# Kernel tuning notes

Hardware: AMD Instinct MI355X
Metric: run time of the kernel (lower is better)

## Reference

```python
import jax, jax.numpy as jnp
import numpy as np

VOCAB = 32000
DIM = 1024
N_BLOCKS = 5
L_CONST = 1e9


def setup_inputs() -> dict:
    key = jax.random.key(0)
    k1, k2, k3, k4, k5, k6 = jax.random.split(key, 6)
    x = jax.random.normal(k1, (2, 2048, DIM), dtype=jnp.float32)
    gates_w = jax.random.uniform(k2, (VOCAB, 1), dtype=jnp.float32)  # mimics uniform_(0.001, 1.0)
    weight = jax.random.normal(k3, (DIM, VOCAB), dtype=jnp.float32) * 0.02
    bias = jax.random.normal(k4, (VOCAB,), dtype=jnp.float32) * 0.02
    blk_w = jax.random.normal(k5, (N_BLOCKS, DIM, DIM), dtype=jnp.float32) * 0.02
    blk_b = jax.random.normal(k6, (N_BLOCKS, DIM), dtype=jnp.float32) * 0.02
    return {"x": x, "gates_w": gates_w, "weight": weight, "bias": bias, "blk_w": blk_w, "blk_b": blk_b}


def reference(x, gates_w, weight, bias, blk_w, blk_b):
    input_dim, vocab = weight.shape  # [D, V]
    gates = gates_w * input_dim  # [V, 1], scaled per-token gate
    idx = jnp.arange(input_dim, dtype=jnp.float32)[None, :]  # [1, D]
    # discrete mask + straight-through residual term (broadcast [V,1] over [V,D])
    mask = (idx < gates).astype(jnp.float32) + (L_CONST * gates - jnp.floor(L_CONST * gates)) / L_CONST  # [V, D]
    masked_weight = weight * mask.T  # [D, V]
    # branch selector per vocab column, in {0,...,4}
    selector = jnp.floor(gates / x.shape[-1] * N_BLOCKS * (1.0 - 1e-10)).reshape(vocab)  # [V]
    ret = jnp.zeros(x.shape[:-1] + (vocab,), dtype=x.dtype)
    for bidx in range(N_BLOCKS):
        x_b = jnp.einsum('bsd,ed->bse', x, blk_w[bidx]) + blk_b[bidx]  # Linear: x @ W^T + b
        temp = jnp.einsum('bsd,dv->bsv', x_b, masked_weight)  # [B, S, V]
        ret = ret + temp * (selector == bidx).astype(jnp.float32)
    return ret + bias
```

## Files before the change

### kernel.cpp

```cpp
#include <hip/hip_runtime.h>
#include <hip/hip_bf16.h>

#define VOCAB 32000
#define DIM 1024
#define NTOK 4096
#define NG 5
#define MAXTILES 255

typedef float f32x4 __attribute__((ext_vector_type(4)));
typedef __bf16 bf16x8 __attribute__((ext_vector_type(8)));

__device__ __forceinline__ unsigned short f2bf(float f) {
    union { float f; unsigned int u; } x; x.f = f;
    unsigned int r = x.u + 0x7fffu + ((x.u >> 16) & 1u);
    return (unsigned short)(r >> 16);
}
__device__ __forceinline__ float bf2f(unsigned short u) {
    union { unsigned int u; float f; } x; x.u = ((unsigned int)u) << 16;
    return x.f;
}

__device__ __forceinline__ void gload16(const void* g, void* l) {
    __builtin_amdgcn_global_load_lds(
        (const __attribute__((address_space(1))) void*)g,
        (__attribute__((address_space(3))) void*)l, 16, 0, 0);
}

__global__ __launch_bounds__(256) void hist_kernel(const float* __restrict__ gates_w,
                                                   int* __restrict__ hist) {
    __shared__ int cnt[NG];
    const int tid = threadIdx.x;
    if (tid < NG) cnt[tid] = 0;
    __syncthreads();
    const int v = blockIdx.x * 256 + tid;
    const int s = min(4, max(0, (int)floorf(gates_w[v] * 5.0f)));
    atomicAdd(&cnt[s], 1);
    __syncthreads();
    if (tid < NG) hist[blockIdx.x * NG + tid] = cnt[tid];
}

__global__ __launch_bounds__(64) void base_kernel(const int* __restrict__ hist,
                                                  int* __restrict__ blkoff,
                                                  int* __restrict__ jlist,
                                                  int4* __restrict__ tdesc,
                                                  int* __restrict__ pbase6) {
    __shared__ int histl[125 * NG];
    __shared__ int cnt[NG], pb[NG], padc[NG];
    const int tid = threadIdx.x;
    for (int i = tid; i < 125 * NG; i += 64) histl[i] = hist[i];
    __syncthreads();
    if (tid == 0) {
        int c[NG] = {0, 0, 0, 0, 0};
        for (int b = 0; b < 125; ++b)
            for (int g = 0; g < NG; ++g) c[g] += histl[b * NG + g];
        const int kmaxs[NG] = {256, 448, 640, 832, 1024};
        int p = 0, t = 0;
        for (int g = 0; g < NG; ++g) {
            pb[g] = p; cnt[g] = c[g];
            padc[g] = ((c[g] + 127) >> 7) << 7;
            pbase6[g] = p;
            p += padc[g];
        }
        pbase6[NG] = p;
        for (int g = 0; g < NG; ++g) {
            int nt = (cnt[g] + 127) >> 7;
            for (int k = 0; k < nt; ++k) { tdesc[t] = make_int4(g, pb[g] + (k << 7), kmaxs[g], 0); ++t; }
        }
        for (; t < MAXTILES; ++t) tdesc[t] = make_int4(-1, 0, 0, 0);
        int run[NG];
        for (int g = 0; g < NG; ++g) run[g] = pb[g];
        for (int b = 0; b < 125; ++b)
            for (int g = 0; g < NG; ++g) { blkoff[b * NG + g] = run[g]; run[g] += histl[b * NG + g]; }
    }
    __syncthreads();
    for (int g = 0; g < NG; ++g)
        for (int i = pb[g] + cnt[g] + tid; i < pb[g] + padc[g]; i += 64) jlist[i] = -1;
}

__global__ __launch_bounds__(256) void place_kernel(const float* __restrict__ gates_w,
                                                    const int* __restrict__ blkoff,
                                                    int* __restrict__ pos,
                                                    int* __restrict__ jlist) {
    __shared__ int wtot[4][NG], wpre[4][NG];
    const int tid = threadIdx.x, lane = tid & 63, wv = tid >> 6;
    const int v = blockIdx.x * 256 + tid;
    const int s = min(4, max(0, (int)floorf(gates_w[v] * 5.0f)));
    int rank = 0;
#pragma unroll
    for (int g = 0; g < NG; ++g) {
        unsigned long long m = __ballot(s == g);
        if (lane == 0) wtot[wv][g] = (int)__popcll(m);
        if (s == g) rank = (int)__popcll(m & ((1ull << lane) - 1ull));
    }
    __syncthreads();
    if (tid < NG) {
        int a = 0;
        for (int w = 0; w < 4; ++w) { wpre[w][tid] = a; a += wtot[w][tid]; }
    }
    __syncthreads();
    const int p = blkoff[blockIdx.x * NG + s] + wpre[wv][s] + rank;
    pos[v] = p;
    jlist[p] = v;
}

__global__ void conv_kernel(const float* __restrict__ in, unsigned short* __restrict__ out, int n4) {
    int i = blockIdx.x * blockDim.x + threadIdx.x;
    if (i >= n4) return;
    const float4 f = ((const float4*)in)[i];
    ushort4 o;
    o.x = f2bf(f.x); o.y = f2bf(f.y); o.z = f2bf(f.z); o.w = f2bf(f.w);
    ((ushort4*)out)[i] = o;
}

__global__ __launch_bounds__(256) void convT_kernel(const float* __restrict__ blk_w,
                                                    unsigned short* __restrict__ wbfT) {
    __shared__ unsigned short tl[64][68];
    const int i0 = blockIdx.x * 64, o0 = blockIdx.y * 64, g = blockIdx.z;
    const int tid = threadIdx.x;
    const float* src = blk_w + (size_t)g * DIM * DIM;
    unsigned short* dst = wbfT + (size_t)g * DIM * DIM;
#pragma unroll
    for (int it = 0; it < 4; ++it) {
        int idx = it * 256 + tid;
        int lo = idx >> 4;
        int c4 = (idx & 15) * 4;
        float4 w = *(const float4*)&src[(size_t)(o0 + lo) * DIM + i0 + c4];
        tl[c4 + 0][lo] = f2bf(w.x);
        tl[c4 + 1][lo] = f2bf(w.y);
        tl[c4 + 2][lo] = f2bf(w.z);
        tl[c4 + 3][lo] = f2bf(w.w);
    }
    __syncthreads();
#pragma unroll
    for (int it = 0; it < 2; ++it) {
        int idx = it * 256 + tid;
        int ri = idx >> 3, ch = idx & 7;
        union { unsigned short u[8]; uint4 q; } uu;
#pragma unroll
        for (int k = 0; k < 8; ++k) uu.u[k] = tl[ri][ch * 8 + k];
        *(uint4*)(dst + (size_t)(i0 + ri) * DIM + o0 + ch * 8) = uu.q;
    }
}

__global__ __launch_bounds__(256) void wm_kernel(const float* __restrict__ weight,
                                                 const float* __restrict__ gates_w,
                                                 const int* __restrict__ pos,
                                                 unsigned short* __restrict__ wmbp) {
    __shared__ unsigned short tl[64][68];
    __shared__ float gatev[64];
    __shared__ int posv[64];
    const int v0 = blockIdx.x * 64, d0 = blockIdx.y * 64;
    const int tid = threadIdx.x;
    if (tid < 64) { gatev[tid] = gates_w[v0 + tid] * 1024.0f; posv[tid] = pos[v0 + tid]; }
    __syncthreads();
#pragma unroll
    for (int it = 0; it < 4; ++it) {
        int idx = it * 256 + tid;
        int ld = idx >> 4;
        int c4 = (idx & 15) * 4;
        const float dv = (float)(d0 + ld);
        float4 w = *(const float4*)&weight[(size_t)(d0 + ld) * VOCAB + v0 + c4];
        tl[c4 + 0][ld] = f2bf((dv < gatev[c4 + 0]) ? w.x : 0.0f);
        tl[c4 + 1][ld] = f2bf((dv < gatev[c4 + 1]) ? w.y : 0.0f);
        tl[c4 + 2][ld] = f2bf((dv < gatev[c4 + 2]) ? w.z : 0.0f);
        tl[c4 + 3][ld] = f2bf((dv < gatev[c4 + 3]) ? w.w : 0.0f);
    }
    __syncthreads();
#pragma unroll
    for (int it = 0; it < 2; ++it) {
        int idx = it * 256 + tid;
        int lv = idx >> 3, ch = idx & 7;
        union { unsigned short u[8]; uint4 q; } uu;
#pragma unroll
        for (int k = 0; k < 8; ++k) uu.u[k] = tl[lv][ch * 8 + k];
        *(uint4*)(wmbp + (size_t)posv[lv] * DIM + d0 + ch * 8) = uu.q;
    }
}

__global__ __launch_bounds__(256) void dbias_kernel(const unsigned short* __restrict__ wmbp,
                                                    const float* __restrict__ blk_b,
                                                    const float* __restrict__ bias,
                                                    const int* __restrict__ jlist,
                                                    const int* __restrict__ pbase6,
                                                    float* __restrict__ bias2) {
    const int p = blockIdx.x * 4 + (threadIdx.x >> 6);
    const int lane = threadIdx.x & 63;
    if (p >= pbase6[NG]) return;
    const int v = jlist[p];
    if (v < 0) return;
    int g = 0;
#pragma unroll
    for (int gg = 1; gg < NG; ++gg) if (p >= pbase6[gg]) g = gg;
    const unsigned short* wrow = wmbp + (size_t)p * DIM + lane * 16;
    const float* brow = blk_b + g * DIM + lane * 16;
    union { uint4 q; unsigned short u[8]; } a0, a1;
    a0.q = *(const uint4*)(wrow);
    a1.q = *(const uint4*)(wrow + 8);
    float s = 0.f;
#pragma unroll
    for (int k = 0; k < 8; ++k) s += bf2f(a0.u[k]) * brow[k];
#pragma unroll
    for (int k = 0; k < 8; ++k) s += bf2f(a1.u[k]) * brow[k + 8];
#pragma unroll
    for (int off = 32; off > 0; off >>= 1) s += __shfl_down(s, off);
    if (lane == 0) bias2[v] = bias[v] + s;
}

__global__ __launch_bounds__(256, 2) void ceff_gemm(const unsigned short* __restrict__ wmbp,
                                                    const unsigned short* __restrict__ wbfT,
                                                    const int* __restrict__ jlist,
                                                    const int4* __restrict__ tdesc,
                                                    unsigned short* __restrict__ ceffv) {
    const int4 td = tdesc[blockIdx.x];
    if (td.x < 0) return;
    const int g = td.x, jb = td.y, kmax = td.z;
    const int n0 = blockIdx.y * 128;
    __shared__ __align__(16) unsigned short lA[128 * 64];
    __shared__ __align__(16) unsigned short lB[128 * 64];
    const int tid = threadIdx.x;
    const int lane = tid & 63, wv = tid >> 6;
    const int wm64 = (wv >> 1) * 64, wn64 = (wv & 1) * 64;
    const int lr = lane >> 4, lc = lane & 15;
    f32x4 acc[4][4] = {};
    const int r = tid >> 3, c = tid & 7;
    const unsigned short* sa = wmbp + (size_t)(jb + r) * DIM + c * 8;
    const unsigned short* sb = wbfT + (size_t)g * DIM * DIM + (size_t)(n0 + r) * DIM + c * 8;
    unsigned short* da = &lA[r * 64 + c * 8];
    unsigned short* db = &lB[r * 64 + c * 8];
    const int nkt = kmax >> 6;
    for (int kt = 0; kt < nkt; ++kt) {
#pragma unroll
        for (int s = 0; s < 4; ++s) {
            gload16(sa + (size_t)s * 32 * DIM + kt * 64, da + s * 32 * 64);
            gload16(sb + (size_t)s * 32 * DIM + kt * 64, db + s * 32 * 64);
        }
        __syncthreads();
#pragma unroll
        for (int kk = 0; kk < 64; kk += 32) {
            const int ko = kk + lr * 8;
            bf16x8 af[4], bg[4];
#pragma unroll
            for (int m = 0; m < 4; ++m) af[m] = *(const bf16x8*)&lA[(wm64 + m * 16 + lc) * 64 + ko];
#pragma unroll
            for (int n = 0; n < 4; ++n) bg[n] = *(const bf16x8*)&lB[(wn64 + n * 16 + lc) * 64 + ko];
#pragma unroll
            for (int m = 0; m < 4; ++m)
#pragma unroll
                for (int n = 0; n < 4; ++n)
                    acc[m][n] = __builtin_amdgcn_mfma_f32_16x16x32_bf16(af[m], bg[n], acc[m][n], 0, 0, 0);
        }
        __syncthreads();
    }
#pragma unroll
    for (int m = 0; m < 4; ++m) {
#pragma unroll
        for (int i = 0; i < 4; ++i) {
            const int prow = jb + wm64 + m * 16 + lr * 4 + i;
            const int v = jlist[prow];
            if (v < 0) continue;
#pragma unroll
            for (int n = 0; n < 4; ++n) {
                const int icol = n0 + wn64 + n * 16 + lc;
                ceffv[(size_t)v * DIM + icol] = f2bf(acc[m][n][i]);
            }
        }
    }
}

__global__ __launch_bounds__(256, 4) void out_gemm(const unsigned short* __restrict__ xbf,
                                                   const unsigned short* __restrict__ ceffv,
                                                   const float* __restrict__ bias2,
                                                   float* __restrict__ out) {
    const int rid = blockIdx.y * gridDim.x + blockIdx.x;
    const int swz = (rid & 7) * 1000 + (rid >> 3);
    const int m0 = (swz & 31) * 128;
    const int n0 = (swz >> 5) * 128;
    __shared__ __align__(16) unsigned short lA[128 * 64];
    __shared__ __align__(16) unsigned short lB[128 * 64];
    const int tid = threadIdx.x;
    const int lane = tid & 63, wv = tid >> 6;
    const int wm64 = (wv >> 1) * 64, wn64 = (wv & 1) * 64;
    const int lr = lane >> 4, lc = lane & 15;
    f32x4 acc[4][4] = {};
    const int r = tid >> 3, c = tid & 7;
    const unsigned short* sa = xbf + (size_t)(m0 + r) * DIM + c * 8;
    const unsigned short* sb = ceffv + (size_t)(n0 + r) * DIM + c * 8;
    unsigned short* da = &lA[r * 64 + c * 8];
    unsigned short* db = &lB[r * 64 + c * 8];
    for (int kt = 0; kt < DIM / 64; ++kt) {
#pragma unroll
        for (int s = 0; s < 4; ++s) {
            gload16(sa + (size_t)s * 32 * DIM + kt * 64, da + s * 32 * 64);
            gload16(sb + (size_t)s * 32 * DIM + kt * 64, db + s * 32 * 64);
        }
        __syncthreads();
#pragma unroll
        for (int kk = 0; kk < 64; kk += 32) {
            const int ko = kk + lr * 8;
            bf16x8 af[4], bg[4];
#pragma unroll
            for (int m = 0; m < 4; ++m) af[m] = *(const bf16x8*)&lA[(wm64 + m * 16 + lc) * 64 + ko];
#pragma unroll
            for (int n = 0; n < 4; ++n) bg[n] = *(const bf16x8*)&lB[(wn64 + n * 16 + lc) * 64 + ko];
#pragma unroll
            for (int m = 0; m < 4; ++m)
#pragma unroll
                for (int n = 0; n < 4; ++n)
                    acc[m][n] = __builtin_amdgcn_mfma_f32_16x16x32_bf16(af[m], bg[n], acc[m][n], 0, 0, 0);
        }
        __syncthreads();
    }
#pragma unroll
    for (int n = 0; n < 4; ++n) {
        const int col = n0 + wn64 + n * 16 + lc;
        const float b2 = bias2[col];
#pragma unroll
        for (int m = 0; m < 4; ++m) {
            const int t0 = m0 + wm64 + m * 16 + lr * 4;
#pragma unroll
            for (int i = 0; i < 4; ++i)
                __builtin_nontemporal_store(acc[m][n][i] + b2,
                                            &out[(size_t)(t0 + i) * VOCAB + col]);
        }
    }
}

extern "C" void kernel_launch(void* const* d_in, const int* in_sizes, int n_in,
                              void* d_out, int out_size, void* d_ws, size_t ws_size,
                              hipStream_t stream) {
    const float* x       = (const float*)d_in[0];
    const float* gates_w = (const float*)d_in[1];
    const float* weight  = (const float*)d_in[2];
    const float* bias    = (const float*)d_in[3];
    const float* blk_w   = (const float*)d_in[4];
    const float* blk_b   = (const float*)d_in[5];
    float* out = (float*)d_out;
    char* ws = (char*)d_ws;

    unsigned short* xbf   = (unsigned short*)(ws);
    unsigned short* wbfT  = (unsigned short*)(ws + 8388608);
    unsigned short* wmbp  = (unsigned short*)(ws + 18874368);
    unsigned short* ceffv = (unsigned short*)(ws + 85721088);
    float* bias2 = (float*)(ws + 151257088);
    int*   pos   = (int*)(ws + 151385088);
    int*   jlist = (int*)(ws + 151513088);
    int4*  tdesc = (int4*)(ws + 151643648);
    int*   pbase6 = (int*)(ws + 151647728);
    int*   hist   = (int*)(ws + 151647752);
    int*   blkoff = (int*)(ws + 151650252);

    hist_kernel<<<dim3(125), dim3(256), 0, stream>>>(gates_w, hist);
    base_kernel<<<dim3(1), dim3(64), 0, stream>>>(hist, blkoff, jlist, tdesc, pbase6);
    place_kernel<<<dim3(125), dim3(256), 0, stream>>>(gates_w, blkoff, pos, jlist);
    conv_kernel<<<dim3(4096), dim3(256), 0, stream>>>(x, xbf, 1048576);
    convT_kernel<<<dim3(16, 16, NG), dim3(256), 0, stream>>>(blk_w, wbfT);
    wm_kernel<<<dim3(500, 16), dim3(256), 0, stream>>>(weight, gates_w, pos, wmbp);
    dbias_kernel<<<dim3(8160), dim3(256), 0, stream>>>(wmbp, blk_b, bias, jlist, pbase6, bias2);
    ceff_gemm<<<dim3(MAXTILES, 8), dim3(256), 0, stream>>>(wmbp, wbfT, jlist, tdesc, ceffv);
    out_gemm<<<dim3(250, 32), dim3(256), 0, stream>>>(xbf, ceffv, bias2, out);
}
```

Before: 1.031 ms.

## Rewrite out_gemm as 256x256 tile with double-buffered 8-wave LDS pipeline

Replaces the 128x128-tile output GEMM, which loaded and waited within each k-step, with a 256x256 tile computed by 512 threads. Global-to-LDS loads of half-k slices are double-buffered and issued in phases interleaved with MFMA work, using explicit vmcnt waits, barriers and setprio. An XCD-aware block mapping assigns tiles to blocks. This aims to hide load latency and raise arithmetic intensity per LDS byte, at the cost of 128KB of LDS, more accumulator registers and fewer resident blocks.

```diff
diff --git a/kernel.cpp b/kernel.cpp
--- a/kernel.cpp
+++ b/kernel.cpp
@@ -267,59 +267,109 @@
     }
 }
 
-__global__ __launch_bounds__(256, 4) void out_gemm(const unsigned short* __restrict__ xbf,
+#define BARRIER() do { asm volatile("" ::: "memory"); \
+    __builtin_amdgcn_s_barrier(); asm volatile("" ::: "memory"); } while (0)
+#define WAITV4() do { asm volatile("s_waitcnt vmcnt(4)" ::: "memory"); \
+    __builtin_amdgcn_sched_barrier(0); } while (0)
+#define WAITV0() do { asm volatile("s_waitcnt vmcnt(0)" ::: "memory"); \
+    __builtin_amdgcn_sched_barrier(0); } while (0)
+
+__global__ __launch_bounds__(512, 2) void out_gemm(const unsigned short* __restrict__ xbf,
                                                    const unsigned short* __restrict__ ceffv,
                                                    const float* __restrict__ bias2,
                                                    float* __restrict__ out) {
-    const int rid = blockIdx.y * gridDim.x + blockIdx.x;
-    const int swz = (rid & 7) * 1000 + (rid >> 3);
-    const int m0 = (swz & 31) * 128;
-    const int n0 = (swz >> 5) * 128;
-    __shared__ __align__(16) unsigned short lA[128 * 64];
-    __shared__ __align__(16) unsigned short lB[128 * 64];
-    const int tid = threadIdx.x;
-    const int lane = tid & 63, wv = tid >> 6;
-    const int wm64 = (wv >> 1) * 64, wn64 = (wv & 1) * 64;
-    const int lr = lane >> 4, lc = lane & 15;
-    f32x4 acc[4][4] = {};
-    const int r = tid >> 3, c = tid & 7;
-    const unsigned short* sa = xbf + (size_t)(m0 + r) * DIM + c * 8;
-    const unsigned short* sb = ceffv + (size_t)(n0 + r) * DIM + c * 8;
-    unsigned short* da = &lA[r * 64 + c * 8];
-    unsigned short* db = &lB[r * 64 + c * 8];
-    for (int kt = 0; kt < DIM / 64; ++kt) {
-#pragma unroll
-        for (int s = 0; s < 4; ++s) {
-            gload16(sa + (size_t)s * 32 * DIM + kt * 64, da + s * 32 * 64);
-            gload16(sb + (size_t)s * 32 * DIM + kt * 64, db + s * 32 * 64);
-        }
-        __syncthreads();
-#pragma unroll
-        for (int kk = 0; kk < 64; kk += 32) {
-            const int ko = kk + lr * 8;
-            bf16x8 af[4], bg[4];
-#pragma unroll
-            for (int m = 0; m < 4; ++m) af[m] = *(const bf16x8*)&lA[(wm64 + m * 16 + lc) * 64 + ko];
-#pragma unroll
-            for (int n = 0; n < 4; ++n) bg[n] = *(const bf16x8*)&lB[(wn64 + n * 16 + lc) * 64 + ko];
-#pragma unroll
-            for (int m = 0; m < 4; ++m)
-#pragma unroll
-                for (int n = 0; n < 4; ++n)
-                    acc[m][n] = __builtin_amdgcn_mfma_f32_16x16x32_bf16(af[m], bg[n], acc[m][n], 0, 0, 0);
-        }
-        __syncthreads();
-    }
-#pragma unroll
-    for (int n = 0; n < 4; ++n) {
-        const int col = n0 + wn64 + n * 16 + lc;
-        const float b2 = bias2[col];
-#pragma unroll
-        for (int m = 0; m < 4; ++m) {
-            const int t0 = m0 + wm64 + m * 16 + lr * 4;
+    const int rid = blockIdx.x;
+    const int c = rid & 7, l = rid >> 3;
+    const int m0 = (c * 2 + (l & 1)) * 256;
+    const int n0 = (l >> 1) * 256;
+    __shared__ __align__(16) unsigned short lds[65536];
+    const int tid = threadIdx.x;
+    const int wv = tid >> 6, lane = tid & 63;
+    const int wm = wv >> 2, wn = wv & 3;
+    const int lc = lane & 15, lr = lane >> 4;
+    f32x4 acc[8][4] = {};
+    bf16x8 bg[4];
+
+    auto STAGE_A = [&](int t, int h, int b) {
+#pragma unroll
+        for (int j = 0; j < 2; ++j) {
+            const int fi = j * 512 + tid;
+            const int r = fi >> 2, kc8 = (fi & 3) * 8;
+            gload16(xbf + (size_t)(m0 + r) * DIM + t * 64 + h * 32 + kc8,
+                    &lds[(b * 2 + h) * 8192 + fi * 8]);
+        }
+    };
+    auto STAGE_B = [&](int t, int h, int b) {
+#pragma unroll
+        for (int j = 0; j < 2; ++j) {
+            const int fi = j * 512 + tid;
+            const int r = fi >> 2, kc8 = (fi & 3) * 8;
+            gload16(ceffv + (size_t)(n0 + r) * DIM + t * 64 + h * 32 + kc8,
+                    &lds[32768 + (b * 2 + h) * 8192 + fi * 8]);
+        }
+    };
+
+#define PHASE(mq, h, b, DO_B, STAGE_STMT, WAIT_STMT)                                   \
+    {                                                                                   \
+        const unsigned short* Ah = &lds[((b) * 2 + (h)) * 8192];                        \
+        const unsigned short* Bh = &lds[32768 + ((b) * 2 + (h)) * 8192];                \
+        bf16x8 af[4];                                                                   \
+        _Pragma("unroll")                                                               \
+        for (int mf = 0; mf < 4; ++mf)                                                  \
+            af[mf] = *(const bf16x8*)&Ah[(wm * 128 + (mq) * 64 + mf * 16 + lc) * 32 + lr * 8]; \
+        if (DO_B) {                                                                     \
+            _Pragma("unroll")                                                           \
+            for (int nf = 0; nf < 4; ++nf)                                              \
+                bg[nf] = *(const bf16x8*)&Bh[(wn * 64 + nf * 16 + lc) * 32 + lr * 8];   \
+        }                                                                               \
+        STAGE_STMT;                                                                     \
+        BARRIER();                                                                      \
+        __builtin_amdgcn_s_setprio(1);                                                  \
+        _Pragma("unroll")                                                               \
+        for (int mf = 0; mf < 4; ++mf)                                                  \
+            _Pragma("unroll")                                                           \
+            for (int nf = 0; nf < 4; ++nf)                                              \
+                acc[(mq) * 4 + mf][nf] = __builtin_amdgcn_mfma_f32_16x16x32_bf16(       \
+                    af[mf], bg[nf], acc[(mq) * 4 + mf][nf], 0, 0, 0);                   \
+        __builtin_amdgcn_s_setprio(0);                                                  \
+        WAIT_STMT;                                                                      \
+        BARRIER();                                                                      \
+    }
+
+    STAGE_A(0, 0, 0); STAGE_B(0, 0, 0);
+    STAGE_A(0, 1, 0); STAGE_B(0, 1, 0);
+    STAGE_A(1, 0, 1); STAGE_B(1, 0, 1);
+    WAITV0();
+    BARRIER();
+
+    for (int t = 0; t < 14; ++t) {
+        const int b = t & 1, nb = b ^ 1;
+        PHASE(0, 0, b, true,  STAGE_A(t + 1, 1, nb), );
+        PHASE(1, 0, b, false, STAGE_B(t + 1, 1, nb), );
+        PHASE(0, 1, b, true,  STAGE_A(t + 2, 0, b), );
+        PHASE(1, 1, b, false, STAGE_B(t + 2, 0, b), WAITV4());
+    }
+    PHASE(0, 0, 0, true,  STAGE_A(15, 1, 1), );
+    PHASE(1, 0, 0, false, STAGE_B(15, 1, 1), );
+    PHASE(0, 1, 0, true,  , );
+    PHASE(1, 1, 0, false, , WAITV0());
+    PHASE(0, 0, 1, true,  , );
+    PHASE(1, 0, 1, false, , );
+    PHASE(0, 1, 1, true,  , );
+    PHASE(1, 1, 1, false, , );
+
+#undef PHASE
+
+#pragma unroll
+    for (int am = 0; am < 8; ++am) {
+#pragma unroll
+        for (int nf = 0; nf < 4; ++nf) {
+            const int col = n0 + wn * 64 + nf * 16 + lc;
+            const float b2 = bias2[col];
+            const int t0 = m0 + wm * 128 + am * 16 + lr * 4;
 #pragma unroll
             for (int i = 0; i < 4; ++i)
-                __builtin_nontemporal_store(acc[m][n][i] + b2,
+                __builtin_nontemporal_store(acc[am][nf][i] + b2,
                                             &out[(size_t)(t0 + i) * VOCAB + col]);
         }
     }
@@ -357,5 +407,5 @@
     wm_kernel<<<dim3(500, 16), dim3(256), 0, stream>>>(weight, gates_w, pos, wmbp);
     dbias_kernel<<<dim3(8160), dim3(256), 0, stream>>>(wmbp, blk_b, bias, jlist, pbase6, bias2);
     ceff_gemm<<<dim3(MAXTILES, 8), dim3(256), 0, stream>>>(wmbp, wbfT, jlist, tdesc, ceffv);
-    out_gemm<<<dim3(250, 32), dim3(256), 0, stream>>>(xbf, ceffv, bias2, out);
-}
+    out_gemm<<<dim3(2000), dim3(512), 0, stream>>>(xbf, ceffv, bias2, out);
+}
```

Result: faster. 990.0 us (-4.0%).
